# Kernel tuning notes

Measured on AMD Instinct MI355X. Metric: run time of the kernel, lower is better.

## Reference

```python
import jax, jax.numpy as jnp
import numpy as np

NUM_LAYERS = 32
IN_SIZE = 1024
OUT_SIZE = 1024
B, S = 32, 256


def setup_inputs() -> dict:
    key = jax.random.key(0)
    k1, k2, k3 = jax.random.split(key, 3)
    x = jax.random.normal(k1, (B, S, IN_SIZE), dtype=jnp.float32)
    layer_idx = jax.random.randint(k2, (S,), 0, NUM_LAYERS, dtype=jnp.int32)
    # learned parameter: per-layer weight [L, O, D], normal(stddev=1.0) as in flax init
    weight = jax.random.normal(k3, (NUM_LAYERS, OUT_SIZE, IN_SIZE), dtype=jnp.float32)
    return {"x": x, "layer_idx": layer_idx, "weight": weight}


def reference(x, layer_idx, weight):
    # x: [B, S, D]; layer_idx: [S]; weight: [L, O, D]
    # Each sequence position s uses expert weight[layer_idx[s]]:
    #   out[b, s, o] = sum_d x[b, s, d] * weight[layer_idx[s], o, d]
    w = weight[layer_idx]                      # [S, O, D] gather
    return jnp.einsum('bsd,sod->bso', x, w)    # [B, S, O]
```

## Files before the change

### kernel.cpp

```cpp
#include <hip/hip_runtime.h>
#include <stdint.h>

#define NLAYERS 32
#define DSIZE   1024
#define OSIZE   1024
#define BATCH   32
#define SEQ     256

#define WS_PERM  16
#define WS_TILE  512
#define MAX_TILES 88
#define NSPLIT   16

typedef __attribute__((ext_vector_type(8)))  short short8;
typedef __attribute__((ext_vector_type(16))) float f32x16;

#define LDSTRIDE 72
#define BK 64

static __device__ __forceinline__ void lds_barrier() {
    asm volatile("s_waitcnt lgkmcnt(0)\n\ts_barrier" ::: "memory");
}

__global__ void prep_kernel(const int* __restrict__ layer_idx, int* __restrict__ wsi) {
    __shared__ int cnt[NLAYERS];
    __shared__ int start_[NLAYERS];
    __shared__ int cursor[NLAYERS];
    const int t = threadIdx.x;
    if (t < NLAYERS) cnt[t] = 0;
    __syncthreads();
    int l = 0;
    if (t < SEQ) { l = layer_idx[t]; atomicAdd(&cnt[l], 1); }
    __syncthreads();
    if (t == 0) {
        int acc = 0;
        for (int i = 0; i < NLAYERS; ++i) { start_[i] = acc; cursor[i] = acc; acc += cnt[i]; }
    }
    __syncthreads();
    if (t < SEQ) {
        int r = atomicAdd(&cursor[l], 1);
        wsi[WS_PERM + r] = t;
    }
    if (t == 0) {
        int nt = 0;
        for (int i = 0; i < NLAYERS; ++i) {
            const int c = cnt[i];
            for (int j = 0; j < c; j += 4) {
                wsi[WS_TILE + nt*4 + 0] = i;
                wsi[WS_TILE + nt*4 + 1] = start_[i] + j;
                wsi[WS_TILE + nt*4 + 2] = (c - j < 4) ? (c - j) : 4;
                ++nt;
            }
        }
        wsi[0] = nt;
    }
}

static __device__ __forceinline__ unsigned pk2(float a, float b) {
    unsigned ua = __builtin_bit_cast(unsigned, a) + 0x8000u;
    unsigned ub = __builtin_bit_cast(unsigned, b) + 0x8000u;
    return __builtin_amdgcn_perm(ub, ua, 0x07060302u);
}

__global__ __launch_bounds__(512, 7) void gemm_kernel(
        const float* __restrict__ x, const float* __restrict__ wgt,
        const int* __restrict__ wsi, float* __restrict__ out) {
    const int ntiles = wsi[0];
    const int xcd = blockIdx.x & 7;
    const int idx = blockIdx.x >> 3;
    const int g_lo = (xcd * ntiles) >> 3;
    const int g_hi = ((xcd + 1) * ntiles) >> 3;
    const int nblk = (g_hi - g_lo) << 4;
    if (idx >= nblk) return;
    const int mt    = g_lo + (idx >> 4);
    const int ntile = idx & 15;
    const int layer     = wsi[WS_TILE + mt*4 + 0];
    const int rank_base = wsi[WS_TILE + mt*4 + 1];
    const int nranks    = wsi[WS_TILE + mt*4 + 2];

    __shared__ __align__(16) short ldsA[128 * LDSTRIDE];
    __shared__ __align__(16) short ldsB[64 * LDSTRIDE];

    const int t     = threadIdx.x;
    const int c4    = (t & 15) * 4;
    const int rbase = t >> 4;

    int sv[4];
    #pragma unroll
    for (int j = 0; j < 4; ++j)
        sv[j] = (j < nranks) ? wsi[WS_PERM + rank_base + j] : 0;

    const float* abase = x + (((size_t)(rbase * SEQ)) << 10) + c4;
    const float* bptr = wgt + (((size_t)((layer << 10) + ntile * 64 + rbase)) << 10) + c4;

    float4 ra[4], rb[2];
    auto load_step = [&](int kk) {
        #pragma unroll
        for (int p = 0; p < 4; ++p) {
            if (p < nranks) ra[p] = *(const float4*)(abase + ((size_t)sv[p] << 10) + kk);
            else            ra[p] = make_float4(0.f, 0.f, 0.f, 0.f);
        }
        #pragma unroll
        for (int p = 0; p < 2; ++p)
            rb[p] = *(const float4*)(bptr + ((size_t)p << 15) + kk);
    };

    const int lane = t & 63;
    const int wv   = t >> 6;
    const int ro   = wv >> 1;
    const int nh   = wv & 1;
    const int l31  = lane & 31;
    const int lh   = lane >> 5;

    f32x16 acc;
    #pragma unroll
    for (int r = 0; r < 16; ++r) acc[r] = 0.f;

    const short* pA0 = &ldsA[(ro * 32 + l31) * LDSTRIDE + lh * 8];
    const short* pB0 = &ldsB[(nh * 32 + l31) * LDSTRIDE + lh * 8];

    load_step(0);
    #pragma unroll 1
    for (int kk = 0; kk < DSIZE; kk += BK) {
        lds_barrier();
        #pragma unroll
        for (int p = 0; p < 4; ++p) {
            const int row = rbase + 32 * p;
            uint2 va;
            va.x = pk2(ra[p].x, ra[p].y);
            va.y = pk2(ra[p].z, ra[p].w);
            *(uint2*)&ldsA[row * LDSTRIDE + c4] = va;
        }
        #pragma unroll
        for (int p = 0; p < 2; ++p) {
            const int row = rbase + 32 * p;
            uint2 vb;
            vb.x = pk2(rb[p].x, rb[p].y);
            vb.y = pk2(rb[p].z, rb[p].w);
            *(uint2*)&ldsB[row * LDSTRIDE + c4] = vb;
        }
        if (kk + BK < DSIZE) load_step(kk + BK);
        lds_barrier();
        #pragma unroll
        for (int sub = 0; sub < 4; ++sub) {
            short8 a0 = *(const short8*)(pA0 + sub*16);
            short8 b0 = *(const short8*)(pB0 + sub*16);
            acc = __builtin_amdgcn_mfma_f32_32x32x16_bf16(a0, b0, acc, 0, 0, 0);
        }
    }

    if (ro < nranks) {
        const int s = wsi[WS_PERM + rank_base + ro];
        const int ocol = ntile * 64 + nh * 32 + l31;
        #pragma unroll
        for (int r = 0; r < 16; ++r) {
            const int brow = (r & 3) + 8 * (r >> 2) + 4 * lh;
            out[(((size_t)(brow * SEQ + s)) << 10) + ocol] = acc[r];
        }
    }
}

extern "C" void kernel_launch(void* const* d_in, const int* in_sizes, int n_in,
                              void* d_out, int out_size, void* d_ws, size_t ws_size,
                              hipStream_t stream) {
    const float* x         = (const float*)d_in[0];
    const int*   layer_idx = (const int*)  d_in[1];
    const float* weight    = (const float*)d_in[2];
    float* out = (float*)d_out;
    int*   wsi = (int*)d_ws;

    prep_kernel<<<1, 256, 0, stream>>>(layer_idx, wsi);
    gemm_kernel<<<MAX_TILES * NSPLIT, 512, 0, stream>>>(x, weight, wsi, out);
}
```

Baseline: 259.5 us.

## Stream fp32 tiles directly into double-buffered LDS with global_load_lds

Result: slower. 286.6 us (+10.5%).

```diff
diff --git a/kernel.cpp b/kernel.cpp
--- a/kernel.cpp
+++ b/kernel.cpp
@@ -12,15 +12,12 @@
 #define MAX_TILES 88
 #define NSPLIT   16
 
+#define BK   32
+#define NIT  (DSIZE / BK)
+#define THREADS 512
+
 typedef __attribute__((ext_vector_type(8)))  short short8;
 typedef __attribute__((ext_vector_type(16))) float f32x16;
-
-#define LDSTRIDE 72
-#define BK 64
-
-static __device__ __forceinline__ void lds_barrier() {
-    asm volatile("s_waitcnt lgkmcnt(0)\n\ts_barrier" ::: "memory");
-}
 
 __global__ void prep_kernel(const int* __restrict__ layer_idx, int* __restrict__ wsi) {
     __shared__ int cnt[NLAYERS];
@@ -62,7 +59,13 @@
     return __builtin_amdgcn_perm(ub, ua, 0x07060302u);
 }
 
-__global__ __launch_bounds__(512, 7) void gemm_kernel(
+static __device__ __forceinline__ void gload16(const float* g, float* l) {
+    __builtin_amdgcn_global_load_lds(
+        (const __attribute__((address_space(1))) void*)g,
+        (__attribute__((address_space(3))) void*)l, 16, 0, 0);
+}
+
+__global__ __launch_bounds__(THREADS, 6) void gemm_kernel(
         const float* __restrict__ x, const float* __restrict__ wgt,
         const int* __restrict__ wsi, float* __restrict__ out) {
     const int ntiles = wsi[0];
@@ -78,75 +81,74 @@
     const int rank_base = wsi[WS_TILE + mt*4 + 1];
     const int nranks    = wsi[WS_TILE + mt*4 + 2];
 
-    __shared__ __align__(16) short ldsA[128 * LDSTRIDE];
-    __shared__ __align__(16) short ldsB[64 * LDSTRIDE];
+    __shared__ __align__(16) float ldsA[2][128 * BK];
+    __shared__ __align__(16) float ldsB[2][64 * BK];
 
-    const int t     = threadIdx.x;
-    const int c4    = (t & 15) * 4;
-    const int rbase = t >> 4;
-
-    int sv[4];
-    #pragma unroll
-    for (int j = 0; j < 4; ++j)
-        sv[j] = (j < nranks) ? wsi[WS_PERM + rank_base + j] : 0;
-
-    const float* abase = x + (((size_t)(rbase * SEQ)) << 10) + c4;
-    const float* bptr = wgt + (((size_t)((layer << 10) + ntile * 64 + rbase)) << 10) + c4;
-
-    float4 ra[4], rb[2];
-    auto load_step = [&](int kk) {
-        #pragma unroll
-        for (int p = 0; p < 4; ++p) {
-            if (p < nranks) ra[p] = *(const float4*)(abase + ((size_t)sv[p] << 10) + kk);
-            else            ra[p] = make_float4(0.f, 0.f, 0.f, 0.f);
-        }
-        #pragma unroll
-        for (int p = 0; p < 2; ++p)
-            rb[p] = *(const float4*)(bptr + ((size_t)p << 15) + kk);
-    };
-
+    const int t    = threadIdx.x;
     const int lane = t & 63;
     const int wv   = t >> 6;
-    const int ro   = wv >> 1;
-    const int nh   = wv & 1;
     const int l31  = lane & 31;
     const int lh   = lane >> 5;
+
+    const int swzf = ((lane & 7) ^ (lane >> 3)) << 2;
+
+    const int riA = wv >> 1;
+    const int sW  = (riA < nranks) ? wsi[WS_PERM + rank_base + riA] : 0;
+    const int b0  = ((wv & 1) << 4) + (lane >> 3);
+    const float* aptr0 = x + (((size_t)(b0 * SEQ + sW)) << 10) + swzf;
+    const float* aptr1 = aptr0 + ((size_t)8 * SEQ << 10);
+    const int rB0 = ntile * 64 + wv * 8 + (lane >> 3);
+    const float* bptr = wgt + ((size_t)layer << 20) + (((size_t)rB0) << 10) + swzf;
+
+    float* dA = &ldsA[0][0] + wv * 16 * BK;
+    float* dB = &ldsB[0][0] + wv * 8 * BK;
+
+    const int ro  = wv >> 1;
+    const int nh  = wv & 1;
+    const int rsw = l31 & 7;
+    const int oA  = (ro * 32 + l31) * BK;
+    const int oB  = (nh * 32 + l31) * BK;
 
     f32x16 acc;
     #pragma unroll
     for (int r = 0; r < 16; ++r) acc[r] = 0.f;
 
-    const short* pA0 = &ldsA[(ro * 32 + l31) * LDSTRIDE + lh * 8];
-    const short* pB0 = &ldsB[(nh * 32 + l31) * LDSTRIDE + lh * 8];
+    gload16(aptr0, dA);
+    gload16(aptr1, dA + 8 * BK);
+    gload16(bptr,  dB);
 
-    load_step(0);
     #pragma unroll 1
-    for (int kk = 0; kk < DSIZE; kk += BK) {
-        lds_barrier();
+    for (int kt = 0; kt < NIT; ++kt) {
+        const int c = kt & 1;
+        if (kt + 1 < NIT) {
+            const int kn = (kt + 1) * BK;
+            const int nb = (c ^ 1);
+            gload16(aptr0 + kn, dA + nb * 128 * BK);
+            gload16(aptr1 + kn, dA + nb * 128 * BK + 8 * BK);
+            gload16(bptr  + kn, dB + nb * 64 * BK);
+            asm volatile("s_waitcnt vmcnt(3)\n\ts_barrier" ::: "memory");
+        } else {
+            asm volatile("s_waitcnt vmcnt(0)\n\ts_barrier" ::: "memory");
+        }
+        const float* pa = &ldsA[c][oA];
+        const float* pb = &ldsB[c][oB];
         #pragma unroll
-        for (int p = 0; p < 4; ++p) {
-            const int row = rbase + 32 * p;
-            uint2 va;
-            va.x = pk2(ra[p].x, ra[p].y);
-            va.y = pk2(ra[p].z, ra[p].w);
-            *(uint2*)&ldsA[row * LDSTRIDE + c4] = va;
+        for (int sub = 0; sub < 2; ++sub) {
+            const int g0 = 4 * sub + 2 * lh;
+            float4 alo = *(const float4*)&pa[((g0    ) ^ rsw) << 2];
+            float4 ahi = *(const float4*)&pa[((g0 + 1) ^ rsw) << 2];
+            float4 blo = *(const float4*)&pb[((g0    ) ^ rsw) << 2];
+            float4 bhi = *(const float4*)&pb[((g0 + 1) ^ rsw) << 2];
+            uint4 ua, ub;
+            ua.x = pk2(alo.x, alo.y); ua.y = pk2(alo.z, alo.w);
+            ua.z = pk2(ahi.x, ahi.y); ua.w = pk2(ahi.z, ahi.w);
+            ub.x = pk2(blo.x, blo.y); ub.y = pk2(blo.z, blo.w);
+            ub.z = pk2(bhi.x, bhi.y); ub.w = pk2(bhi.z, bhi.w);
+            short8 a0 = __builtin_bit_cast(short8, ua);
+            short8 bb = __builtin_bit_cast(short8, ub);
+            acc = __builtin_amdgcn_mfma_f32_32x32x16_bf16(a0, bb, acc, 0, 0, 0);
         }
-        #pragma unroll
-        for (int p = 0; p < 2; ++p) {
-            const int row = rbase + 32 * p;
-            uint2 vb;
-            vb.x = pk2(rb[p].x, rb[p].y);
-            vb.y = pk2(rb[p].z, rb[p].w);
-            *(uint2*)&ldsB[row * LDSTRIDE + c4] = vb;
-        }
-        if (kk + BK < DSIZE) load_step(kk + BK);
-        lds_barrier();
-        #pragma unroll
-        for (int sub = 0; sub < 4; ++sub) {
-            short8 a0 = *(const short8*)(pA0 + sub*16);
-            short8 b0 = *(const short8*)(pB0 + sub*16);
-            acc = __builtin_amdgcn_mfma_f32_32x32x16_bf16(a0, b0, acc, 0, 0, 0);
-        }
+        asm volatile("s_waitcnt lgkmcnt(0)\n\ts_barrier" ::: "memory");
     }
 
     if (ro < nranks) {
@@ -170,5 +172,5 @@
     int*   wsi = (int*)d_ws;
 
     prep_kernel<<<1, 256, 0, stream>>>(layer_idx, wsi);
-    gemm_kernel<<<MAX_TILES * NSPLIT, 512, 0, stream>>>(x, weight, wsi, out);
+    gemm_kernel<<<MAX_TILES * NSPLIT, THREADS, 0, stream>>>(x, weight, wsi, out);
 }
```
